# Kernel optimization log

Measured on AMD Instinct MI355X. Metric: run time of the kernel, lower is better.

Reference implementation:

```python
import jax, jax.numpy as jnp
from jax import lax
import numpy as np

B, N, C = 8, 16384, 3   # batch, points per cloud, xyz channels
G, S, TD = 512, 32, 384  # num groups, group size, token_dim


def setup_inputs() -> dict:
    key = jax.random.key(0)
    ks = jax.random.split(key, 8)
    return {
        "points": jax.random.normal(ks[0], (B, N, C), jnp.float32),
        "lengths": jnp.full((B,), N, dtype=jnp.int32),
        # MiniPointNet params (Conv1d kernel-size-1 == per-point matmul)
        "w1": jax.random.normal(ks[1], (128, C), jnp.float32) * 0.1,   # conv1 (no bias)
        "g1": jnp.ones((128,), jnp.float32), "be1": jnp.zeros((128,), jnp.float32),  # BN1
        "w2": jax.random.normal(ks[2], (256, 128), jnp.float32) * 0.05, "b2": jnp.zeros((256,), jnp.float32),
        "w3": jax.random.normal(ks[3], (512, 512), jnp.float32) * 0.03,  # conv3 (no bias)
        "g3": jnp.ones((512,), jnp.float32), "be3": jnp.zeros((512,), jnp.float32),  # BN2
        "w4": jax.random.normal(ks[4], (TD, 512), jnp.float32) * 0.03, "b4": jnp.zeros((TD,), jnp.float32),
    }


def _fps(pts, num_groups):
    # farthest point sampling: sequential over G, vectorized over B,N
    Bb, Nn, _ = pts.shape
    idx0 = jnp.zeros((Bb, num_groups), jnp.int32)
    mind0 = jnp.full((Bb, Nn), 1e10, pts.dtype)
    last0 = pts[:, 0]  # start from point 0

    def body(i, carry):
        idx, mind, last = carry
        d = jnp.sum((pts - last[:, None, :]) ** 2, axis=-1)  # [B,N]
        mind = jnp.minimum(mind, d)
        nxt = jnp.argmax(mind, axis=1).astype(jnp.int32)     # [B]
        idx = idx.at[:, i].set(nxt)
        last = jnp.take_along_axis(pts, nxt[:, None, None], axis=1)[:, 0]
        return idx, mind, last

    idx, _, _ = lax.fori_loop(1, num_groups, body, (idx0, mind0, last0))
    return idx  # [B,G]


def _bn(x, g, b, eps=1e-5):
    # training-mode BatchNorm1d over (batch*group, point) dims; x: [M,S,ch]
    m = jnp.mean(x, axis=(0, 1))
    v = jnp.var(x, axis=(0, 1))
    return (x - m) * (g * lax.rsqrt(v + eps)) + b


def _mini_pointnet(x, w1, g1, be1, w2, b2, w3, g3, be3, w4, b4):
    # x: [M,S,C] ; 1x1 convs are matmuls over the channel dim
    f = x @ w1.T                              # [M,S,128]
    f = jax.nn.relu(_bn(f, g1, be1))
    f = f @ w2.T + b2                         # [M,S,256]
    fg = jnp.max(f, axis=1, keepdims=True)    # [M,1,256]
    f = jnp.concatenate([jnp.broadcast_to(fg, f.shape), f], axis=-1)  # [M,S,512]
    f = f @ w3.T                              # [M,S,512]
    f = jax.nn.relu(_bn(f, g3, be3))
    f = f @ w4.T + b4                         # [M,S,TD]
    return jnp.max(f, axis=1)                 # [M,TD]


def reference(points, lengths, w1, g1, be1, w2, b2, w3, g3, be3, w4, b4):
    # grouping: FPS centers + KNN neighborhoods, centered on group center
    c_idx = _fps(points, G)                                   # [B,G]
    centers = jnp.take_along_axis(points, c_idx[:, :, None], axis=1)  # [B,G,3]
    d = jnp.sum((centers[:, :, None, :] - points[:, None, :, :]) ** 2, axis=-1)  # [B,G,N]
    knn = lax.top_k(-d, S)[1]                                 # [B,G,S] nearest indices
    group = jax.vmap(lambda p, i: p[i])(points, knn)          # [B,G,S,C] irregular gather
    group = group - centers[:, :, None, :]                    # relative coords
    tokens = _mini_pointnet(group.reshape(B * G, S, C),
                            w1, g1, be1, w2, b2, w3, g3, be3, w4, b4).reshape(B, G, TD)
    embedding_mask = jnp.ones((B, G), bool)  # lengths == N, all groups valid
    return tokens, centers, embedding_mask
```

## Files before the change

### kernel.cpp

```cpp
#include <hip/hip_runtime.h>
#include <hip/hip_bf16.h>
#include <cstdint>

#define NB 8
#define NP 16384
#define NG 512
#define NS 32
#define TDM 384
#define BGT (NB*NG)
#define NR (BGT*NS)
#define C1 128
#define C2 256
#define C3 512

typedef __attribute__((ext_vector_type(8))) short bfrag;
typedef __attribute__((ext_vector_type(4))) float facc;
typedef __attribute__((ext_vector_type(2))) float f32x2;

__device__ __forceinline__ ushort f2bf(float f) {
  uint32_t u = __float_as_uint(f);
  uint32_t r = (u + 0x7FFFu + ((u >> 16) & 1u)) >> 16;
  return (ushort)r;
}
__device__ __forceinline__ float bf2f(ushort h) {
  return __uint_as_float(((uint32_t)h) << 16);
}

__device__ __forceinline__ void gld_lds16(const void* g, void* l) {
  __builtin_amdgcn_global_load_lds(
      (const __attribute__((address_space(1))) void*)g,
      (__attribute__((address_space(3))) void*)l, 16, 0, 0);
}

#define OFF_CIDX   0u
#define OFF_CENT   16384u
#define OFF_GROUP  65536u
#define OFF_XPART  1638400u
#define OFF_BN1    1785856u
#define OFF_BN3    1786880u
#define OFF_W2B    1790976u
#define OFF_W3BB   1856512u
#define OFF_W4B    2118656u
#define OFF_FG     2511872u
#define OFF_FGP    6706176u
#define OFF_PART   15094784u
#define OFF_F2     19289088u

template <int PHASE>
__global__ __launch_bounds__(512, 2) void k_fps(const float* __restrict__ pts,
                                                int* __restrict__ cidx,
                                                float* __restrict__ centers,
                                                float* __restrict__ outc,
                                                float* __restrict__ mstate,
                                                const float* __restrict__ w2,
                                                const float* __restrict__ w3,
                                                const float* __restrict__ w4,
                                                ushort* __restrict__ w2b,
                                                ushort* __restrict__ w3bb,
                                                ushort* __restrict__ w4b,
                                                float* __restrict__ mask) {
#pragma clang fp contract(off)
  const int t = threadIdx.x;
  if (PHASE == 0 && blockIdx.x >= NB) {
    int i = (blockIdx.x - NB) * 512 + t;
    if (i < 32768) {
      int r = i >> 7, c = i & 127;
      w2b[i] = f2bf(w2[r * 128 + c]);
    } else if (i < 163840) {
      int j = i - 32768; int r = j >> 8, c = j & 255;
      w3bb[j] = f2bf(w3[(size_t)r * 512 + 256 + c]);
    } else if (i < 360448) {
      int j = i - 163840; int r = j >> 9, c = j & 511;
      w4b[j] = f2bf(w4[(size_t)r * 512 + c]);
    } else if (i < 364544) {
      mask[i - 360448] = 1.0f;
    }
    return;
  }
  const int b = blockIdx.x;
  const float* P = pts + (size_t)b * NP * 3;
  f32x2 px[16], py[16], pz[16], m[16];
#pragma unroll
  for (int k = 0; k < 16; k++) {
    int p0 = (2 * k) * 512 + t;
    int p1 = p0 + 512;
    px[k] = (f32x2){P[p0 * 3 + 0], P[p1 * 3 + 0]};
    py[k] = (f32x2){P[p0 * 3 + 1], P[p1 * 3 + 1]};
    pz[k] = (f32x2){P[p0 * 3 + 2], P[p1 * 3 + 2]};
    if (PHASE == 0) {
      m[k] = (f32x2){1e10f, 1e10f};
    } else {
      m[k].x = mstate[(size_t)(b * 32 + 2 * k) * 512 + t];
      m[k].y = mstate[(size_t)(b * 32 + 2 * k + 1) * 512 + t];
    }
  }
  __shared__ double kb[2][8];
  float cx, cy, cz;
  if (PHASE == 0) {
    cx = P[0]; cy = P[1]; cz = P[2];
    if (t == 0) {
      cidx[b * NG] = 0;
      size_t o = (size_t)b * NG * 3;
      centers[o] = cx; centers[o + 1] = cy; centers[o + 2] = cz;
      outc[o] = cx; outc[o + 1] = cy; outc[o + 2] = cz;
    }
  } else {
    size_t o = ((size_t)b * NG + (PHASE * 128 - 1)) * 3;
    cx = centers[o]; cy = centers[o + 1]; cz = centers[o + 2];
  }
  const unsigned nt = ~(unsigned)t;
  const int i_beg = (PHASE == 0) ? 1 : PHASE * 128;
  const int i_end = (PHASE + 1) * 128;
  for (int i = i_beg; i < i_end; i++) {
    const int par = i & 1;
    const f32x2 ccx = (f32x2){cx, cx};
    const f32x2 ccy = (f32x2){cy, cy};
    const f32x2 ccz = (f32x2){cz, cz};
    double A = 0.0, B = 0.0;
#pragma unroll
    for (int k = 0; k < 16; k++) {
      f32x2 dx = px[k] - ccx;
      f32x2 dy = py[k] - ccy;
      f32x2 dz = pz[k] - ccz;
      f32x2 d = (dx * dx + dy * dy) + dz * dz;
      f32x2 mm = __builtin_elementwise_min(m[k], d);
      m[k] = mm;
      unsigned lo0 = nt - (unsigned)(2 * k) * 512u;
      unsigned lo1 = nt - (unsigned)(2 * k + 1) * 512u;
      double k0 = __longlong_as_double(((unsigned long long)__float_as_uint(mm.x) << 32) | lo0);
      double k1 = __longlong_as_double(((unsigned long long)__float_as_uint(mm.y) << 32) | lo1);
      A = fmax(A, k0);
      B = fmax(B, k1);
    }
    double best = fmax(A, B);
#pragma unroll
    for (int off = 1; off < 64; off <<= 1)
      best = fmax(best, __shfl_xor(best, off));
    if ((t & 63) == 0) kb[par][t >> 6] = best;
    __syncthreads();
    double v0 = fmax(kb[par][0], kb[par][1]);
    double v1 = fmax(kb[par][2], kb[par][3]);
    double v2 = fmax(kb[par][4], kb[par][5]);
    double v3 = fmax(kb[par][6], kb[par][7]);
    const double g = fmax(fmax(v0, v1), fmax(v2, v3));
    const int gidx = (int)(~(unsigned)__double_as_longlong(g));
    const float* q = P + (size_t)gidx * 3;
    cx = q[0]; cy = q[1]; cz = q[2];
    if (t == 0) {
      cidx[b * NG + i] = gidx;
      size_t o = ((size_t)b * NG + i) * 3;
      centers[o] = cx; centers[o + 1] = cy; centers[o + 2] = cz;
      outc[o] = cx; outc[o + 1] = cy; outc[o + 2] = cz;
    }
  }
  if (PHASE < 3) {
#pragma unroll
    for (int k = 0; k < 16; k++) {
      mstate[(size_t)(b * 32 + 2 * k) * 512 + t] = m[k].x;
      mstate[(size_t)(b * 32 + 2 * k + 1) * 512 + t] = m[k].y;
    }
  }
}

__device__ __forceinline__ unsigned wave_iscan(unsigned v, int lane) {
#pragma unroll
  for (int s = 1; s < 64; s <<= 1) {
    unsigned o = (unsigned)__shfl_up((int)v, s);
    if (lane >= s) v += o;
  }
  return v;
}

__global__ __launch_bounds__(512) void k_knn(const float* __restrict__ pts,
                                             const float* __restrict__ centers,
                                             float* __restrict__ group,
                                             float* __restrict__ xpart) {
  __shared__ uint32_t h1[4][257];
  __shared__ uint32_t h2[4][257];
  __shared__ int cand_i[1024];
  __shared__ float cand_v[1024];
  __shared__ int sel[32];
  __shared__ float selc[96];
  __shared__ unsigned wsum[4];
  __shared__ int cnts[8];
  __shared__ float redv[8];
  __shared__ int redi[8];
  const int t = threadIdx.x;
  const int lane = t & 63;
  const int cp = lane & 3;
  const int bg = blockIdx.x;
  const int b = bg >> 9;
  const float* P = pts + (size_t)b * NP * 3;
  const float cx = centers[bg * 3], cy = centers[bg * 3 + 1], cz = centers[bg * 3 + 2];
  float dl[32];
#pragma unroll
  for (int rr = 0; rr < NP / 512; rr++) {
    int p = rr * 512 + t;
    float dx = __fsub_rn(P[p * 3], cx);
    float dy = __fsub_rn(P[p * 3 + 1], cy);
    float dz = __fsub_rn(P[p * 3 + 2], cz);
    dl[rr] = __fadd_rn(__fadd_rn(__fmul_rn(dx, dx), __fmul_rn(dy, dy)), __fmul_rn(dz, dz));
  }
  for (int u = t; u < 4 * 257; u += 512) { h1[0][u] = 0; h2[0][u] = 0; }
  if (t < 8) cnts[t] = 0;
  __syncthreads();
#pragma unroll
  for (int rr = 0; rr < NP / 512; rr++)
    atomicAdd(&h1[cp][__float_as_uint(dl[rr]) >> 23], 1u);
  __syncthreads();
  unsigned v1 = 0, i1 = 0;
  if (t < 256) {
    v1 = h1[0][t] + h1[1][t] + h1[2][t] + h1[3][t];
    i1 = wave_iscan(v1, lane);
    if (lane == 63) wsum[t >> 6] = i1;
  }
  __syncthreads();
  if (t < 256) {
    unsigned off = 0;
    for (int q = 0; q < (t >> 6); q++) off += wsum[q];
    unsigned incl = i1 + off, excl = incl - v1;
    if (incl >= NS && excl < NS) { cnts[2] = t; cnts[3] = (int)excl; }
  }
  __syncthreads();
  const uint32_t e1 = (uint32_t)cnts[2];
  const int lt0 = cnts[3];
#pragma unroll
  for (int rr = 0; rr < NP / 512; rr++) {
    uint32_t bits = __float_as_uint(dl[rr]);
    if ((bits >> 23) == e1) atomicAdd(&h2[cp][(bits >> 15) & 255u], 1u);
  }
  __syncthreads();
  unsigned v2 = 0, i2 = 0;
  if (t < 256) {
    v2 = h2[0][t] + h2[1][t] + h2[2][t] + h2[3][t];
    i2 = wave_iscan(v2, lane);
    if (lane == 63) wsum[t >> 6] = i2;
  }
  __syncthreads();
  if (t < 256) {
    unsigned off = 0;
    for (int q = 0; q < (t >> 6); q++) off += wsum[q];
    unsigned incl = (unsigned)lt0 + i2 + off, excl = incl - v2;
    if (incl >= NS && excl < NS) { cnts[4] = t; cnts[5] = (int)excl; }
  }
  __syncthreads();
  const uint32_t keystar = (e1 << 8) | (uint32_t)cnts[4];
  const int lt = cnts[5];
#pragma unroll
  for (int rr = 0; rr < NP / 512; rr++) {
    int p = rr * 512 + t;
    uint32_t key = __float_as_uint(dl[rr]) >> 15;
    if (key < keystar) { int pos = atomicAdd(&cnts[0], 1); sel[pos] = p; }
    else if (key == keystar) {
      int pos = atomicAdd(&cnts[1], 1);
      if (pos < 1024) { cand_i[pos] = p; cand_v[pos] = dl[rr]; }
    }
  }
  __syncthreads();
  const int neq = cnts[1];
  if (neq <= 1024) {
    const int need = NS - lt;
    for (int e = t; e < neq; e += 512) {
      int p = cand_i[e];
      float v = cand_v[e];
      int rank = 0;
      for (int q = 0; q < neq; q++) {
        int pq = cand_i[q];
        float vq = cand_v[q];
        rank += (vq < v || (vq == v && pq < p)) ? 1 : 0;
      }
      if (rank < need) sel[lt + rank] = p;
    }
    __syncthreads();
  } else {
    uint32_t taken = 0;
    for (int j = 0; j < NS; j++) {
      float bv = 3.4e38f; int bp = 0x7FFFFFFF;
#pragma unroll
      for (int rr = 0; rr < NP / 512; rr++) {
        if (!((taken >> rr) & 1u)) {
          float v = dl[rr];
          int p = rr * 512 + t;
          if (v < bv || (v == bv && p < bp)) { bv = v; bp = p; }
        }
      }
#pragma unroll
      for (int off = 32; off >= 1; off >>= 1) {
        float ov = __shfl_xor(bv, off);
        int   op = __shfl_xor(bp, off);
        if (ov < bv || (ov == bv && op < bp)) { bv = ov; bp = op; }
      }
      if (lane == 0) { redv[t >> 6] = bv; redi[t >> 6] = bp; }
      __syncthreads();
      float fv = redv[0]; int fp = redi[0];
      for (int q = 1; q < 8; q++)
        if (redv[q] < fv || (redv[q] == fv && redi[q] < fp)) { fv = redv[q]; fp = redi[q]; }
      if (t == (fp & 511)) taken |= 1u << (fp >> 9);
      if (t == 0) sel[j] = fp;
      __syncthreads();
    }
  }
  if (t < NS) {
    int p = sel[t];
    float gx = __fsub_rn(P[p * 3], cx);
    float gy = __fsub_rn(P[p * 3 + 1], cy);
    float gz = __fsub_rn(P[p * 3 + 2], cz);
    size_t row = ((size_t)bg * NS + t) * 3;
    group[row] = gx; group[row + 1] = gy; group[row + 2] = gz;
    selc[t * 3] = gx; selc[t * 3 + 1] = gy; selc[t * 3 + 2] = gz;
  }
  __syncthreads();
  if (t < 32) {
    float x = selc[t * 3], y = selc[t * 3 + 1], z = selc[t * 3 + 2];
    float s0 = x, s1 = y, s2 = z;
    float s3 = x * x, s4 = y * y, s5 = z * z;
    float s6 = x * y, s7 = x * z, s8 = y * z;
#pragma unroll
    for (int off = 16; off >= 1; off >>= 1) {
      s0 += __shfl_xor(s0, off); s1 += __shfl_xor(s1, off); s2 += __shfl_xor(s2, off);
      s3 += __shfl_xor(s3, off); s4 += __shfl_xor(s4, off); s5 += __shfl_xor(s5, off);
      s6 += __shfl_xor(s6, off); s7 += __shfl_xor(s7, off); s8 += __shfl_xor(s8, off);
    }
    if (t == 0) {
      float* xp = xpart + (size_t)bg * 9;
      xp[0]=s0; xp[1]=s1; xp[2]=s2; xp[3]=s3; xp[4]=s4; xp[5]=s5; xp[6]=s6; xp[7]=s7; xp[8]=s8;
    }
  }
}

__global__ __launch_bounds__(256) void k_bn1(const float* __restrict__ xpart,
                                             const float* __restrict__ w1,
                                             const float* __restrict__ g1,
                                             const float* __restrict__ be1,
                                             float* __restrict__ bn1) {
  __shared__ float wsum[4][9];
  __shared__ float S[9];
  const int t = threadIdx.x;
  float s[9];
#pragma unroll
  for (int j = 0; j < 9; j++) s[j] = 0.f;
  for (int i = t; i < BGT; i += 256) {
    const float* xp = xpart + (size_t)i * 9;
#pragma unroll
    for (int j = 0; j < 9; j++) s[j] += xp[j];
  }
#pragma unroll
  for (int off = 32; off >= 1; off >>= 1)
#pragma unroll
    for (int j = 0; j < 9; j++) s[j] += __shfl_xor(s[j], off);
  if ((t & 63) == 0)
#pragma unroll
    for (int j = 0; j < 9; j++) wsum[t >> 6][j] = s[j];
  __syncthreads();
  if (t == 0)
#pragma unroll
    for (int j = 0; j < 9; j++) S[j] = wsum[0][j] + wsum[1][j] + wsum[2][j] + wsum[3][j];
  __syncthreads();
  if (t < C1) {
    const float rn = 1.0f / (float)NR;
    float ex = S[0]*rn, ey = S[1]*rn, ez = S[2]*rn;
    float exx = S[3]*rn, eyy = S[4]*rn, ezz = S[5]*rn;
    float exy = S[6]*rn, exz = S[7]*rn, eyz = S[8]*rn;
    float a = w1[t*3], b = w1[t*3+1], c = w1[t*3+2];
    float mean = a*ex + b*ey + c*ez;
    float e2 = a*a*exx + b*b*eyy + c*c*ezz + 2.f*(a*b*exy + a*c*exz + b*c*eyz);
    float var = e2 - mean*mean;
    float sc = g1[t] / sqrtf(var + 1e-5f);
    bn1[t*2] = sc;
    bn1[t*2+1] = be1[t] - mean*sc;
  }
}

#define L12_LDS 102400
__global__ __launch_bounds__(512) void k_l12(const float* __restrict__ group,
                                             const float* __restrict__ w1,
                                             const float* __restrict__ bn1,
                                             const ushort* __restrict__ w2b,
                                             const float* __restrict__ b2,
                                             ushort* __restrict__ f2,
                                             float* __restrict__ fg) {
  extern __shared__ char sm[];
  float* xr = (float*)sm;
  float* a1s1 = (float*)(sm + 1536);
  char* f1A = sm + 4096;
  char* w2B = sm + 36864;
  char* f2s = sm + 4096;
  const int t = threadIdx.x;
  const int mb = blockIdx.x;
  const size_t R0 = (size_t)mb * 128;
  if (t < 384) xr[t] = group[R0 * 3 + t];
  if (t < 256) a1s1[t] = bn1[t];
  for (int u = t; u < 4096; u += 512) {
    int row = u >> 4, c = u & 15;
    gld_lds16((const int4*)w2b + (row * 16 + (c ^ (row & 7))), w2B + u * 16);
  }
  __syncthreads();
  {
    const int c = t & 127;
    const int rb = t >> 7;
    const float wa = w1[c*3], wb = w1[c*3+1], wc = w1[c*3+2];
    const float a1 = a1s1[c*2], s1 = a1s1[c*2+1];
#pragma unroll 4
    for (int i = 0; i < 32; i++) {
      int r = rb * 32 + i;
      float f = xr[r*3] * wa + xr[r*3+1] * wb + xr[r*3+2] * wc;
      float h = fmaxf(fmaf(f, a1, s1), 0.0f);
      *(ushort*)(f1A + r * 256 + ((c * 2) ^ ((r & 7) << 4))) = f2bf(h);
    }
  }
  __syncthreads();
  const int l = t & 63, w = t >> 6;
  const int wm = w >> 2, wn = w & 3;
  const int lr = l & 15, lh = l >> 4;
  facc acc[4][4];
#pragma unroll
  for (int tm = 0; tm < 4; tm++)
#pragma unroll
    for (int tn = 0; tn < 4; tn++) acc[tm][tn] = (facc)0.0f;
#pragma unroll
  for (int ks = 0; ks < 4; ks++) {
    const int kb = (ks * 32 + lh * 8) * 2;
    bfrag af[4], bf[4];
#pragma unroll
    for (int tm = 0; tm < 4; tm++) {
      int row = wm * 64 + tm * 16 + lr;
      af[tm] = *(const bfrag*)(f1A + row * 256 + (kb ^ ((row & 7) << 4)));
    }
#pragma unroll
    for (int tn = 0; tn < 4; tn++) {
      int rn = wn * 64 + tn * 16 + lr;
      bf[tn] = *(const bfrag*)(w2B + rn * 256 + (kb ^ ((rn & 7) << 4)));
    }
#pragma unroll
    for (int tm = 0; tm < 4; tm++)
#pragma unroll
      for (int tn = 0; tn < 4; tn++)
        acc[tm][tn] = __builtin_amdgcn_mfma_f32_16x16x32_bf16(af[tm], bf[tn], acc[tm][tn], 0, 0, 0);
  }
  __syncthreads();
#pragma unroll
  for (int tn = 0; tn < 4; tn++) {
    int col = wn * 64 + tn * 16 + lr;
    float bb = b2[col];
#pragma unroll
    for (int tm = 0; tm < 4; tm++)
#pragma unroll
      for (int r = 0; r < 4; r++) {
        int row = wm * 64 + tm * 16 + lh * 4 + r;
        *(ushort*)(f2s + row * 512 + ((col * 2) ^ ((row & 7) << 4))) = f2bf(acc[tm][tn][r] + bb);
      }
  }
  __syncthreads();
  for (int u = t; u < 4096; u += 512) {
    int row = u >> 5, cu = u & 31;
    int4 v = *(const int4*)(f2s + row * 512 + ((cu * 16) ^ ((row & 7) << 4)));
    ((int4*)(f2 + R0 * 256))[u] = v;
  }
  for (int task = t; task < 1024; task += 512) {
    int g = task >> 8, c = task & 255;
    float mx = -3.4e38f;
#pragma unroll 8
    for (int r = 0; r < 32; r++) {
      int row = g * 32 + r;
      mx = fmaxf(mx, bf2f(*(const ushort*)(f2s + row * 512 + ((c * 2) ^ ((row & 7) << 4)))));
    }
    fg[(size_t)(mb * 4 + g) * 256 + c] = mx;
  }
}

__global__ __launch_bounds__(256) void k_fgpart(const float* __restrict__ fg,
                                                const float* __restrict__ w3,
                                                float* __restrict__ fgpart) {
  __shared__ float fgs[16 * 256];
  const int t = threadIdx.x;
  const int g0 = blockIdx.x * 16;
  for (int i = t; i < 4096; i += 256) fgs[i] = fg[(size_t)g0 * 256 + i];
  __syncthreads();
  for (int half = 0; half < 2; half++) {
    int n = half * 256 + t;
    const float* wr = w3 + (size_t)n * 512;
    float acc[16];
#pragma unroll
    for (int r = 0; r < 16; r++) acc[r] = 0.f;
    for (int k = 0; k < 256; k++) {
      float wv = wr[k];
#pragma unroll
      for (int r = 0; r < 16; r++) acc[r] = fmaf(fgs[r * 256 + k], wv, acc[r]);
    }
#pragma unroll
    for (int r = 0; r < 16; r++) fgpart[(size_t)(g0 + r) * 512 + n] = acc[r];
  }
}

#define L34S_LDS 133120
#define L34O_LDS 163840
template <int OUT>
__global__ __launch_bounds__(512) void k_l34(const ushort* __restrict__ f2,
                                             const ushort* __restrict__ w3bb,
                                             const ushort* __restrict__ w4b,
                                             const float* __restrict__ fgpart,
                                             const float* __restrict__ bn3,
                                             const float* __restrict__ b4,
                                             float* __restrict__ partials,
                                             float* __restrict__ tokens) {
  extern __shared__ char sm[];
  char* Al = sm;
  char* Bl = sm + 65536;
  char* Hl = sm + 131072;
  float* st = (float*)(sm + 131072);
  const int t = threadIdx.x;
  const int mb = blockIdx.x;
  const size_t R0 = (size_t)mb * 128;
  const int g0 = mb * 4;
  const int l = t & 63, w = t >> 6;
  const int wm = w >> 2, wn = w & 3;
  const int lr = l & 15, lh = l >> 4;
  for (int u = t; u < 4096; u += 512) {
    int row = u >> 5, c = u & 31;
    gld_lds16((const int4*)(f2 + R0 * 256) + (row * 32 + (c ^ (row & 7))), Al + u * 16);
  }
  facc tacc[4][6];
  if (OUT) {
#pragma unroll
    for (int tm = 0; tm < 4; tm++)
#pragma unroll
      for (int tn = 0; tn < 6; tn++) tacc[tm][tn] = (facc)0.0f;
  }
  for (int kc = 0; kc < 4; kc++) {
    for (int u = t; u < 4096; u += 512) {
      int row = u >> 5, c = u & 31;
      gld_lds16((const int4*)(w3bb + (size_t)kc * 128 * 256) + (row * 32 + (c ^ (row & 7))),
                Bl + u * 16);
    }
    __syncthreads();
    facc acc[4][2];
#pragma unroll
    for (int tm = 0; tm < 4; tm++) { acc[tm][0] = (facc)0.0f; acc[tm][1] = (facc)0.0f; }
#pragma unroll
    for (int ks = 0; ks < 8; ks++) {
      const int kb = (ks * 32 + lh * 8) * 2;
      bfrag af[4], bf[2];
#pragma unroll
      for (int tm = 0; tm < 4; tm++) {
        int row = wm * 64 + tm * 16 + lr;
        af[tm] = *(const bfrag*)(Al + row * 512 + (kb ^ ((row & 7) << 4)));
      }
#pragma unroll
      for (int tn = 0; tn < 2; tn++) {
        int rn = wn * 32 + tn * 16 + lr;
        bf[tn] = *(const bfrag*)(Bl + rn * 512 + (kb ^ ((rn & 7) << 4)));
      }
#pragma unroll
      for (int tm = 0; tm < 4; tm++)
#pragma unroll
        for (int tn = 0; tn < 2; tn++)
          acc[tm][tn] = __builtin_amdgcn_mfma_f32_16x16x32_bf16(af[tm], bf[tn], acc[tm][tn], 0, 0, 0);
    }
    float fgp0[2], fgp1[2], a3c[2], s3c[2];
#pragma unroll
    for (int tn = 0; tn < 2; tn++) {
      int col = kc * 128 + wn * 32 + tn * 16 + lr;
      fgp0[tn] = fgpart[(size_t)(g0 + wm * 2) * 512 + col];
      fgp1[tn] = fgpart[(size_t)(g0 + wm * 2 + 1) * 512 + col];
      if (OUT) { a3c[tn] = bn3[col * 2]; s3c[tn] = bn3[col * 2 + 1]; }
    }
    if (OUT == 0) {
      float s1v[2] = {0.f, 0.f}, s2v[2] = {0.f, 0.f};
#pragma unroll
      for (int tm = 0; tm < 4; tm++)
#pragma unroll
        for (int tn = 0; tn < 2; tn++)
#pragma unroll
          for (int r = 0; r < 4; r++) {
            float f3 = acc[tm][tn][r] + (tm < 2 ? fgp0[tn] : fgp1[tn]);
            s1v[tn] += f3; s2v[tn] += f3 * f3;
          }
#pragma unroll
      for (int tn = 0; tn < 2; tn++) {
        s1v[tn] += __shfl_xor(s1v[tn], 16); s1v[tn] += __shfl_xor(s1v[tn], 32);
        s2v[tn] += __shfl_xor(s2v[tn], 16); s2v[tn] += __shfl_xor(s2v[tn], 32);
      }
      if (l < 16) {
#pragma unroll
        for (int tn = 0; tn < 2; tn++) {
          int cl = wn * 32 + tn * 16 + lr;
          st[(wm * 128 + cl) * 2 + 0] = s1v[tn];
          st[(wm * 128 + cl) * 2 + 1] = s2v[tn];
        }
      }
      __syncthreads();
      if (t < 256) {
        int cl = t & 127, s = t >> 7;
        float tot = st[(0 * 128 + cl) * 2 + s] + st[(1 * 128 + cl) * 2 + s];
        partials[(size_t)mb * 1024 + (size_t)(kc * 128 + cl) * 2 + s] = tot;
      }
      __syncthreads();
    } else {
#pragma unroll
      for (int tm = 0; tm < 4; tm++)
#pragma unroll
        for (int tn = 0; tn < 2; tn++)
#pragma unroll
          for (int r = 0; r < 4; r++) {
            int row = wm * 64 + tm * 16 + lh * 4 + r;
            int cl = wn * 32 + tn * 16 + lr;
            float f3 = acc[tm][tn][r] + (tm < 2 ? fgp0[tn] : fgp1[tn]);
            float hv = fmaxf(fmaf(f3, a3c[tn], s3c[tn]), 0.0f);
            *(ushort*)(Hl + row * 256 + ((cl * 2) ^ ((row & 7) << 4))) = f2bf(hv);
          }
      __syncthreads();
#pragma unroll
      for (int p = 0; p < 2; p++) {
        for (int u = t; u < 3072; u += 512) {
          int row = u >> 3, c = u & 7;
          gld_lds16((const int4*)(w4b + (size_t)row * 512 + kc * 128 + p * 64) + (c ^ (row & 7)),
                    Bl + u * 16);
        }
        __syncthreads();
#pragma unroll
        for (int ks = 0; ks < 2; ks++) {
          const int kbh = (p * 64 + ks * 32 + lh * 8) * 2;
          const int kbb = (ks * 32 + lh * 8) * 2;
          bfrag af[4], bf[6];
#pragma unroll
          for (int tm = 0; tm < 4; tm++) {
            int row = wm * 64 + tm * 16 + lr;
            af[tm] = *(const bfrag*)(Hl + row * 256 + (kbh ^ ((row & 7) << 4)));
          }
#pragma unroll
          for (int tn = 0; tn < 6; tn++) {
            int rn = wn * 96 + tn * 16 + lr;
            bf[tn] = *(const bfrag*)(Bl + rn * 128 + (kbb ^ ((rn & 7) << 4)));
          }
#pragma unroll
          for (int tm = 0; tm < 4; tm++)
#pragma unroll
            for (int tn = 0; tn < 6; tn++)
              tacc[tm][tn] = __builtin_amdgcn_mfma_f32_16x16x32_bf16(af[tm], bf[tn], tacc[tm][tn], 0, 0, 0);
        }
        __syncthreads();
      }
    }
  }
  if (OUT) {
#pragma unroll
    for (int tn = 0; tn < 6; tn++) {
      int col = wn * 96 + tn * 16 + lr;
      float bb = b4[col];
#pragma unroll
      for (int half = 0; half < 2; half++) {
        float mx = -3.4e38f;
#pragma unroll
        for (int tm = half * 2; tm < half * 2 + 2; tm++)
#pragma unroll
          for (int r = 0; r < 4; r++) mx = fmaxf(mx, tacc[tm][tn][r]);
        mx = fmaxf(mx, __shfl_xor(mx, 16));
        mx = fmaxf(mx, __shfl_xor(mx, 32));
        if (l < 16) tokens[(size_t)(g0 + wm * 2 + half) * TDM + col] = mx + bb;
      }
    }
  }
}

__global__ __launch_bounds__(1024) void k_bn3(const float* __restrict__ partials,
                                              const float* __restrict__ g3,
                                              const float* __restrict__ be3,
                                              float* __restrict__ bn3) {
  __shared__ float ls[128][8];
  const int t = threadIdx.x;
  const int slot_l = t & 127;
  const int chunk = t >> 7;
  const int slot = blockIdx.x * 128 + slot_l;
  float s = 0.f;
  for (int m = chunk * 128; m < chunk * 128 + 128; m++)
    s += partials[(size_t)m * 1024 + slot];
  ls[slot_l][chunk] = s;
  __syncthreads();
  if (t < 64) {
    int col = blockIdx.x * 64 + t;
    float s1 = 0.f, s2 = 0.f;
#pragma unroll
    for (int c = 0; c < 8; c++) { s1 += ls[2 * t][c]; s2 += ls[2 * t + 1][c]; }
    const float rn = 1.0f / (float)NR;
    float mean = s1 * rn;
    float var = s2 * rn - mean * mean;
    float a = g3[col] / sqrtf(var + 1e-5f);
    bn3[col * 2] = a;
    bn3[col * 2 + 1] = be3[col] - mean * a;
  }
}

extern "C" void kernel_launch(void* const* d_in, const int* in_sizes, int n_in,
                              void* d_out, int out_size, void* d_ws, size_t ws_size,
                              hipStream_t stream) {
  const float* points = (const float*)d_in[0];
  const float* w1 = (const float*)d_in[2];
  const float* g1 = (const float*)d_in[3];
  const float* be1 = (const float*)d_in[4];
  const float* w2 = (const float*)d_in[5];
  const float* b2 = (const float*)d_in[6];
  const float* w3 = (const float*)d_in[7];
  const float* g3 = (const float*)d_in[8];
  const float* be3 = (const float*)d_in[9];
  const float* w4 = (const float*)d_in[10];
  const float* b4 = (const float*)d_in[11];
  char* ws = (char*)d_ws;
  int* cidx = (int*)(ws + OFF_CIDX);
  float* centers = (float*)(ws + OFF_CENT);
  float* group = (float*)(ws + OFF_GROUP);
  float* xpart = (float*)(ws + OFF_XPART);
  float* bn1 = (float*)(ws + OFF_BN1);
  float* bn3 = (float*)(ws + OFF_BN3);
  ushort* w2b = (ushort*)(ws + OFF_W2B);
  ushort* w3bb = (ushort*)(ws + OFF_W3BB);
  ushort* w4b = (ushort*)(ws + OFF_W4B);
  float* fg = (float*)(ws + OFF_FG);
  float* fgpart = (float*)(ws + OFF_FGP);
  float* partials = (float*)(ws + OFF_PART);
  ushort* f2 = (ushort*)(ws + OFF_F2);
  float* out = (float*)d_out;
  float* out_centers = out + (size_t)BGT * TDM;
  float* out_mask = out_centers + (size_t)BGT * 3;

  hipFuncSetAttribute((const void*)k_l12, hipFuncAttributeMaxDynamicSharedMemorySize, L12_LDS);
  {
    auto p0 = k_l34<0>; auto p1 = k_l34<1>;
    hipFuncSetAttribute((const void*)p0, hipFuncAttributeMaxDynamicSharedMemorySize, L34S_LDS);
    hipFuncSetAttribute((const void*)p1, hipFuncAttributeMaxDynamicSharedMemorySize, L34O_LDS);
  }

  float* mstate = (float*)(ws + OFF_PART);

  k_fps<0><<<NB + 712, 512, 0, stream>>>(points, cidx, centers, out_centers, mstate,
                                         w2, w3, w4, w2b, w3bb, w4b, out_mask);
  k_fps<1><<<NB, 512, 0, stream>>>(points, cidx, centers, out_centers, mstate,
                                   w2, w3, w4, w2b, w3bb, w4b, out_mask);
  k_fps<2><<<NB, 512, 0, stream>>>(points, cidx, centers, out_centers, mstate,
                                   w2, w3, w4, w2b, w3bb, w4b, out_mask);
  k_fps<3><<<NB, 512, 0, stream>>>(points, cidx, centers, out_centers, mstate,
                                   w2, w3, w4, w2b, w3bb, w4b, out_mask);
  k_knn<<<BGT, 512, 0, stream>>>(points, centers, group, xpart);
  k_bn1<<<1, 256, 0, stream>>>(xpart, w1, g1, be1, bn1);
  k_l12<<<NR / 128, 512, L12_LDS, stream>>>(group, w1, bn1, w2b, b2, f2, fg);
  k_fgpart<<<BGT / 16, 256, 0, stream>>>(fg, w3, fgpart);
  k_l34<0><<<NR / 128, 512, L34S_LDS, stream>>>(f2, w3bb, nullptr, fgpart, nullptr, nullptr, partials, nullptr);
  k_bn3<<<8, 1024, 0, stream>>>(partials, g3, be3, bn3);
  k_l34<1><<<NR / 128, 512, L34O_LDS, stream>>>(f2, w3bb, w4b, fgpart, bn3, b4, nullptr, out);
}
```

Measured before the change: 1.215 ms.

## Overlap KNN grouping with later FPS phases by co-launching blocks

Moves the KNN body into a device function and launches the KNN blocks for the centers chosen in earlier FPS phases as extra blocks inside phases 1-3. The KNN work for groups 0-383 then runs concurrently with the sequential FPS blocks, and only the last 128 groups per batch stay in the standalone k_knn launch. A large dynamic LDS pad is added to the FPS kernels, apparently so that each FPS block gets a compute unit to itself rather than sharing one with KNN blocks. The risk is that the KNN blocks still compete with FPS for memory bandwidth. The scheme also relies on FPS producing centers in 128-center chunks per phase, which earlier phases must complete before the KNN blocks that read them.

```diff
diff --git a/kernel.cpp b/kernel.cpp
--- a/kernel.cpp
+++ b/kernel.cpp
@@ -46,6 +46,171 @@
 #define OFF_PART   15094784u
 #define OFF_F2     19289088u
 
+__device__ __forceinline__ unsigned wave_iscan(unsigned v, int lane) {
+#pragma unroll
+  for (int s = 1; s < 64; s <<= 1) {
+    unsigned o = (unsigned)__shfl_up((int)v, s);
+    if (lane >= s) v += o;
+  }
+  return v;
+}
+
+__device__ void knn_group(int bg, const float* __restrict__ pts,
+                          const float* __restrict__ centers,
+                          float* __restrict__ group,
+                          float* __restrict__ xpart) {
+  __shared__ uint32_t h1[4][257];
+  __shared__ uint32_t h2[4][257];
+  __shared__ int cand_i[1024];
+  __shared__ float cand_v[1024];
+  __shared__ int sel[32];
+  __shared__ float selc[96];
+  __shared__ unsigned wsum[4];
+  __shared__ int cnts[8];
+  __shared__ float redv[8];
+  __shared__ int redi[8];
+  const int t = threadIdx.x;
+  const int lane = t & 63;
+  const int cp = lane & 3;
+  const int b = bg >> 9;
+  const float* P = pts + (size_t)b * NP * 3;
+  const float cx = centers[bg * 3], cy = centers[bg * 3 + 1], cz = centers[bg * 3 + 2];
+  float dl[32];
+#pragma unroll
+  for (int rr = 0; rr < NP / 512; rr++) {
+    int p = rr * 512 + t;
+    float dx = __fsub_rn(P[p * 3], cx);
+    float dy = __fsub_rn(P[p * 3 + 1], cy);
+    float dz = __fsub_rn(P[p * 3 + 2], cz);
+    dl[rr] = __fadd_rn(__fadd_rn(__fmul_rn(dx, dx), __fmul_rn(dy, dy)), __fmul_rn(dz, dz));
+  }
+  for (int u = t; u < 4 * 257; u += 512) { h1[0][u] = 0; h2[0][u] = 0; }
+  if (t < 8) cnts[t] = 0;
+  __syncthreads();
+#pragma unroll
+  for (int rr = 0; rr < NP / 512; rr++)
+    atomicAdd(&h1[cp][__float_as_uint(dl[rr]) >> 23], 1u);
+  __syncthreads();
+  unsigned v1 = 0, i1 = 0;
+  if (t < 256) {
+    v1 = h1[0][t] + h1[1][t] + h1[2][t] + h1[3][t];
+    i1 = wave_iscan(v1, lane);
+    if (lane == 63) wsum[t >> 6] = i1;
+  }
+  __syncthreads();
+  if (t < 256) {
+    unsigned off = 0;
+    for (int q = 0; q < (t >> 6); q++) off += wsum[q];
+    unsigned incl = i1 + off, excl = incl - v1;
+    if (incl >= NS && excl < NS) { cnts[2] = t; cnts[3] = (int)excl; }
+  }
+  __syncthreads();
+  const uint32_t e1 = (uint32_t)cnts[2];
+  const int lt0 = cnts[3];
+#pragma unroll
+  for (int rr = 0; rr < NP / 512; rr++) {
+    uint32_t bits = __float_as_uint(dl[rr]);
+    if ((bits >> 23) == e1) atomicAdd(&h2[cp][(bits >> 15) & 255u], 1u);
+  }
+  __syncthreads();
+  unsigned v2 = 0, i2 = 0;
+  if (t < 256) {
+    v2 = h2[0][t] + h2[1][t] + h2[2][t] + h2[3][t];
+    i2 = wave_iscan(v2, lane);
+    if (lane == 63) wsum[t >> 6] = i2;
+  }
+  __syncthreads();
+  if (t < 256) {
+    unsigned off = 0;
+    for (int q = 0; q < (t >> 6); q++) off += wsum[q];
+    unsigned incl = (unsigned)lt0 + i2 + off, excl = incl - v2;
+    if (incl >= NS && excl < NS) { cnts[4] = t; cnts[5] = (int)excl; }
+  }
+  __syncthreads();
+  const uint32_t keystar = (e1 << 8) | (uint32_t)cnts[4];
+  const int lt = cnts[5];
+#pragma unroll
+  for (int rr = 0; rr < NP / 512; rr++) {
+    int p = rr * 512 + t;
+    uint32_t key = __float_as_uint(dl[rr]) >> 15;
+    if (key < keystar) { int pos = atomicAdd(&cnts[0], 1); sel[pos] = p; }
+    else if (key == keystar) {
+      int pos = atomicAdd(&cnts[1], 1);
+      if (pos < 1024) { cand_i[pos] = p; cand_v[pos] = dl[rr]; }
+    }
+  }
+  __syncthreads();
+  const int neq = cnts[1];
+  if (neq <= 1024) {
+    const int need = NS - lt;
+    for (int e = t; e < neq; e += 512) {
+      int p = cand_i[e];
+      float v = cand_v[e];
+      int rank = 0;
+      for (int q = 0; q < neq; q++) {
+        int pq = cand_i[q];
+        float vq = cand_v[q];
+        rank += (vq < v || (vq == v && pq < p)) ? 1 : 0;
+      }
+      if (rank < need) sel[lt + rank] = p;
+    }
+    __syncthreads();
+  } else {
+    uint32_t taken = 0;
+    for (int j = 0; j < NS; j++) {
+      float bv = 3.4e38f; int bp = 0x7FFFFFFF;
+#pragma unroll
+      for (int rr = 0; rr < NP / 512; rr++) {
+        if (!((taken >> rr) & 1u)) {
+          float v = dl[rr];
+          int p = rr * 512 + t;
+          if (v < bv || (v == bv && p < bp)) { bv = v; bp = p; }
+        }
+      }
+#pragma unroll
+      for (int off = 32; off >= 1; off >>= 1) {
+        float ov = __shfl_xor(bv, off);
+        int   op = __shfl_xor(bp, off);
+        if (ov < bv || (ov == bv && op < bp)) { bv = ov; bp = op; }
+      }
+      if (lane == 0) { redv[t >> 6] = bv; redi[t >> 6] = bp; }
+      __syncthreads();
+      float fv = redv[0]; int fp = redi[0];
+      for (int q = 1; q < 8; q++)
+        if (redv[q] < fv || (redv[q] == fv && redi[q] < fp)) { fv = redv[q]; fp = redi[q]; }
+      if (t == (fp & 511)) taken |= 1u << (fp >> 9);
+      if (t == 0) sel[j] = fp;
+      __syncthreads();
+    }
+  }
+  if (t < NS) {
+    int p = sel[t];
+    float gx = __fsub_rn(P[p * 3], cx);
+    float gy = __fsub_rn(P[p * 3 + 1], cy);
+    float gz = __fsub_rn(P[p * 3 + 2], cz);
+    size_t row = ((size_t)bg * NS + t) * 3;
+    group[row] = gx; group[row + 1] = gy; group[row + 2] = gz;
+    selc[t * 3] = gx; selc[t * 3 + 1] = gy; selc[t * 3 + 2] = gz;
+  }
+  __syncthreads();
+  if (t < 32) {
+    float x = selc[t * 3], y = selc[t * 3 + 1], z = selc[t * 3 + 2];
+    float s0 = x, s1 = y, s2 = z;
+    float s3 = x * x, s4 = y * y, s5 = z * z;
+    float s6 = x * y, s7 = x * z, s8 = y * z;
+#pragma unroll
+    for (int off = 16; off >= 1; off >>= 1) {
+      s0 += __shfl_xor(s0, off); s1 += __shfl_xor(s1, off); s2 += __shfl_xor(s2, off);
+      s3 += __shfl_xor(s3, off); s4 += __shfl_xor(s4, off); s5 += __shfl_xor(s5, off);
+      s6 += __shfl_xor(s6, off); s7 += __shfl_xor(s7, off); s8 += __shfl_xor(s8, off);
+    }
+    if (t == 0) {
+      float* xp = xpart + (size_t)bg * 9;
+      xp[0]=s0; xp[1]=s1; xp[2]=s2; xp[3]=s3; xp[4]=s4; xp[5]=s5; xp[6]=s6; xp[7]=s7; xp[8]=s8;
+    }
+  }
+}
+
 template <int PHASE>
 __global__ __launch_bounds__(512, 2) void k_fps(const float* __restrict__ pts,
                                                 int* __restrict__ cidx,
@@ -58,7 +223,9 @@
                                                 ushort* __restrict__ w2b,
                                                 ushort* __restrict__ w3bb,
                                                 ushort* __restrict__ w4b,
-                                                float* __restrict__ mask) {
+                                                float* __restrict__ mask,
+                                                float* __restrict__ group,
+                                                float* __restrict__ xpart) {
 #pragma clang fp contract(off)
   const int t = threadIdx.x;
   if (PHASE == 0 && blockIdx.x >= NB) {
@@ -75,6 +242,13 @@
     } else if (i < 364544) {
       mask[i - 360448] = 1.0f;
     }
+    return;
+  }
+  if (PHASE >= 1 && blockIdx.x >= NB) {
+    int j = blockIdx.x - NB;
+    int b = j >> 7;
+    int gi = (PHASE - 1) * 128 + (j & 127);
+    knn_group(b * NG + gi, pts, centers, group, xpart);
     return;
   }
   const int b = blockIdx.x;
@@ -162,170 +336,15 @@
   }
 }
 
-__device__ __forceinline__ unsigned wave_iscan(unsigned v, int lane) {
-#pragma unroll
-  for (int s = 1; s < 64; s <<= 1) {
-    unsigned o = (unsigned)__shfl_up((int)v, s);
-    if (lane >= s) v += o;
-  }
-  return v;
-}
-
 __global__ __launch_bounds__(512) void k_knn(const float* __restrict__ pts,
                                              const float* __restrict__ centers,
                                              float* __restrict__ group,
-                                             float* __restrict__ xpart) {
-  __shared__ uint32_t h1[4][257];
-  __shared__ uint32_t h2[4][257];
-  __shared__ int cand_i[1024];
-  __shared__ float cand_v[1024];
-  __shared__ int sel[32];
-  __shared__ float selc[96];
-  __shared__ unsigned wsum[4];
-  __shared__ int cnts[8];
-  __shared__ float redv[8];
-  __shared__ int redi[8];
-  const int t = threadIdx.x;
-  const int lane = t & 63;
-  const int cp = lane & 3;
-  const int bg = blockIdx.x;
-  const int b = bg >> 9;
-  const float* P = pts + (size_t)b * NP * 3;
-  const float cx = centers[bg * 3], cy = centers[bg * 3 + 1], cz = centers[bg * 3 + 2];
-  float dl[32];
-#pragma unroll
-  for (int rr = 0; rr < NP / 512; rr++) {
-    int p = rr * 512 + t;
-    float dx = __fsub_rn(P[p * 3], cx);
-    float dy = __fsub_rn(P[p * 3 + 1], cy);
-    float dz = __fsub_rn(P[p * 3 + 2], cz);
-    dl[rr] = __fadd_rn(__fadd_rn(__fmul_rn(dx, dx), __fmul_rn(dy, dy)), __fmul_rn(dz, dz));
-  }
-  for (int u = t; u < 4 * 257; u += 512) { h1[0][u] = 0; h2[0][u] = 0; }
-  if (t < 8) cnts[t] = 0;
-  __syncthreads();
-#pragma unroll
-  for (int rr = 0; rr < NP / 512; rr++)
-    atomicAdd(&h1[cp][__float_as_uint(dl[rr]) >> 23], 1u);
-  __syncthreads();
-  unsigned v1 = 0, i1 = 0;
-  if (t < 256) {
-    v1 = h1[0][t] + h1[1][t] + h1[2][t] + h1[3][t];
-    i1 = wave_iscan(v1, lane);
-    if (lane == 63) wsum[t >> 6] = i1;
-  }
-  __syncthreads();
-  if (t < 256) {
-    unsigned off = 0;
-    for (int q = 0; q < (t >> 6); q++) off += wsum[q];
-    unsigned incl = i1 + off, excl = incl - v1;
-    if (incl >= NS && excl < NS) { cnts[2] = t; cnts[3] = (int)excl; }
-  }
-  __syncthreads();
-  const uint32_t e1 = (uint32_t)cnts[2];
-  const int lt0 = cnts[3];
-#pragma unroll
-  for (int rr = 0; rr < NP / 512; rr++) {
-    uint32_t bits = __float_as_uint(dl[rr]);
-    if ((bits >> 23) == e1) atomicAdd(&h2[cp][(bits >> 15) & 255u], 1u);
-  }
-  __syncthreads();
-  unsigned v2 = 0, i2 = 0;
-  if (t < 256) {
-    v2 = h2[0][t] + h2[1][t] + h2[2][t] + h2[3][t];
-    i2 = wave_iscan(v2, lane);
-    if (lane == 63) wsum[t >> 6] = i2;
-  }
-  __syncthreads();
-  if (t < 256) {
-    unsigned off = 0;
-    for (int q = 0; q < (t >> 6); q++) off += wsum[q];
-    unsigned incl = (unsigned)lt0 + i2 + off, excl = incl - v2;
-    if (incl >= NS && excl < NS) { cnts[4] = t; cnts[5] = (int)excl; }
-  }
-  __syncthreads();
-  const uint32_t keystar = (e1 << 8) | (uint32_t)cnts[4];
-  const int lt = cnts[5];
-#pragma unroll
-  for (int rr = 0; rr < NP / 512; rr++) {
-    int p = rr * 512 + t;
-    uint32_t key = __float_as_uint(dl[rr]) >> 15;
-    if (key < keystar) { int pos = atomicAdd(&cnts[0], 1); sel[pos] = p; }
-    else if (key == keystar) {
-      int pos = atomicAdd(&cnts[1], 1);
-      if (pos < 1024) { cand_i[pos] = p; cand_v[pos] = dl[rr]; }
-    }
-  }
-  __syncthreads();
-  const int neq = cnts[1];
-  if (neq <= 1024) {
-    const int need = NS - lt;
-    for (int e = t; e < neq; e += 512) {
-      int p = cand_i[e];
-      float v = cand_v[e];
-      int rank = 0;
-      for (int q = 0; q < neq; q++) {
-        int pq = cand_i[q];
-        float vq = cand_v[q];
-        rank += (vq < v || (vq == v && pq < p)) ? 1 : 0;
-      }
-      if (rank < need) sel[lt + rank] = p;
-    }
-    __syncthreads();
-  } else {
-    uint32_t taken = 0;
-    for (int j = 0; j < NS; j++) {
-      float bv = 3.4e38f; int bp = 0x7FFFFFFF;
-#pragma unroll
-      for (int rr = 0; rr < NP / 512; rr++) {
-        if (!((taken >> rr) & 1u)) {
-          float v = dl[rr];
-          int p = rr * 512 + t;
-          if (v < bv || (v == bv && p < bp)) { bv = v; bp = p; }
-        }
-      }
-#pragma unroll
-      for (int off = 32; off >= 1; off >>= 1) {
-        float ov = __shfl_xor(bv, off);
-        int   op = __shfl_xor(bp, off);
-        if (ov < bv || (ov == bv && op < bp)) { bv = ov; bp = op; }
-      }
-      if (lane == 0) { redv[t >> 6] = bv; redi[t >> 6] = bp; }
-      __syncthreads();
-      float fv = redv[0]; int fp = redi[0];
-      for (int q = 1; q < 8; q++)
-        if (redv[q] < fv || (redv[q] == fv && redi[q] < fp)) { fv = redv[q]; fp = redi[q]; }
-      if (t == (fp & 511)) taken |= 1u << (fp >> 9);
-      if (t == 0) sel[j] = fp;
-      __syncthreads();
-    }
-  }
-  if (t < NS) {
-    int p = sel[t];
-    float gx = __fsub_rn(P[p * 3], cx);
-    float gy = __fsub_rn(P[p * 3 + 1], cy);
-    float gz = __fsub_rn(P[p * 3 + 2], cz);
-    size_t row = ((size_t)bg * NS + t) * 3;
-    group[row] = gx; group[row + 1] = gy; group[row + 2] = gz;
-    selc[t * 3] = gx; selc[t * 3 + 1] = gy; selc[t * 3 + 2] = gz;
-  }
-  __syncthreads();
-  if (t < 32) {
-    float x = selc[t * 3], y = selc[t * 3 + 1], z = selc[t * 3 + 2];
-    float s0 = x, s1 = y, s2 = z;
-    float s3 = x * x, s4 = y * y, s5 = z * z;
-    float s6 = x * y, s7 = x * z, s8 = y * z;
-#pragma unroll
-    for (int off = 16; off >= 1; off >>= 1) {
-      s0 += __shfl_xor(s0, off); s1 += __shfl_xor(s1, off); s2 += __shfl_xor(s2, off);
-      s3 += __shfl_xor(s3, off); s4 += __shfl_xor(s4, off); s5 += __shfl_xor(s5, off);
-      s6 += __shfl_xor(s6, off); s7 += __shfl_xor(s7, off); s8 += __shfl_xor(s8, off);
-    }
-    if (t == 0) {
-      float* xp = xpart + (size_t)bg * 9;
-      xp[0]=s0; xp[1]=s1; xp[2]=s2; xp[3]=s3; xp[4]=s4; xp[5]=s5; xp[6]=s6; xp[7]=s7; xp[8]=s8;
-    }
-  }
+                                             float* __restrict__ xpart,
+                                             int gbase) {
+  int j = blockIdx.x;
+  int b = j >> 7;
+  int gi = gbase + (j & 127);
+  knn_group(b * NG + gi, pts, centers, group, xpart);
 }
 
 __global__ __launch_bounds__(256) void k_bn1(const float* __restrict__ xpart,
@@ -689,6 +708,8 @@
     bn3[col * 2 + 1] = be3[col] - mean * a;
   }
 }
+
+#define FPS_PAD 81920
 
 extern "C" void kernel_launch(void* const* d_in, const int* in_sizes, int n_in,
                               void* d_out, int out_size, void* d_ws, size_t ws_size,
@@ -728,18 +749,25 @@
     hipFuncSetAttribute((const void*)p0, hipFuncAttributeMaxDynamicSharedMemorySize, L34S_LDS);
     hipFuncSetAttribute((const void*)p1, hipFuncAttributeMaxDynamicSharedMemorySize, L34O_LDS);
   }
+  {
+    auto f0 = k_fps<0>; auto f1 = k_fps<1>; auto f2k = k_fps<2>; auto f3 = k_fps<3>;
+    hipFuncSetAttribute((const void*)f0, hipFuncAttributeMaxDynamicSharedMemorySize, FPS_PAD);
+    hipFuncSetAttribute((const void*)f1, hipFuncAttributeMaxDynamicSharedMemorySize, FPS_PAD);
+    hipFuncSetAttribute((const void*)f2k, hipFuncAttributeMaxDynamicSharedMemorySize, FPS_PAD);
+    hipFuncSetAttribute((const void*)f3, hipFuncAttributeMaxDynamicSharedMemorySize, FPS_PAD);
+  }
 
   float* mstate = (float*)(ws + OFF_PART);
 
-  k_fps<0><<<NB + 712, 512, 0, stream>>>(points, cidx, centers, out_centers, mstate,
-                                         w2, w3, w4, w2b, w3bb, w4b, out_mask);
-  k_fps<1><<<NB, 512, 0, stream>>>(points, cidx, centers, out_centers, mstate,
-                                   w2, w3, w4, w2b, w3bb, w4b, out_mask);
-  k_fps<2><<<NB, 512, 0, stream>>>(points, cidx, centers, out_centers, mstate,
-                                   w2, w3, w4, w2b, w3bb, w4b, out_mask);
-  k_fps<3><<<NB, 512, 0, stream>>>(points, cidx, centers, out_centers, mstate,
-                                   w2, w3, w4, w2b, w3bb, w4b, out_mask);
-  k_knn<<<BGT, 512, 0, stream>>>(points, centers, group, xpart);
+  k_fps<0><<<NB + 712, 512, FPS_PAD, stream>>>(points, cidx, centers, out_centers, mstate,
+                                               w2, w3, w4, w2b, w3bb, w4b, out_mask, group, xpart);
+  k_fps<1><<<NB + 1024, 512, FPS_PAD, stream>>>(points, cidx, centers, out_centers, mstate,
+                                                w2, w3, w4, w2b, w3bb, w4b, out_mask, group, xpart);
+  k_fps<2><<<NB + 1024, 512, FPS_PAD, stream>>>(points, cidx, centers, out_centers, mstate,
+                                                w2, w3, w4, w2b, w3bb, w4b, out_mask, group, xpart);
+  k_fps<3><<<NB + 1024, 512, FPS_PAD, stream>>>(points, cidx, centers, out_centers, mstate,
+                                                w2, w3, w4, w2b, w3bb, w4b, out_mask, group, xpart);
+  k_knn<<<1024, 512, 0, stream>>>(points, centers, group, xpart, 384);
   k_bn1<<<1, 256, 0, stream>>>(xpart, w1, g1, be1, bn1);
   k_l12<<<NR / 128, 512, L12_LDS, stream>>>(group, w1, bn1, w2b, b2, f2, fg);
   k_fgpart<<<BGT / 16, 256, 0, stream>>>(fg, w3, fgpart);
```

Result: faster. 1.094 ms (-10.0%).
